# Kernel tuning notes

Measured on AMD Instinct MI355X. Metric: run time of the kernel, lower is better.

Reference implementation:

```python
import jax, jax.numpy as jnp
import numpy as np

EPS = 1e-5      # batch-norm epsilon
ALPHA = 0.2     # leaky_relu negative slope


def bn_lrelu(h, gamma, beta):
    # training-mode batch norm over the batch axis, then leaky relu
    mean = jnp.mean(h, axis=0)
    var = jnp.var(h, axis=0)
    h = (h - mean) * jax.lax.rsqrt(var + EPS) * gamma + beta
    return jnp.where(h >= 0, h, ALPHA * h)


def setup_inputs() -> dict:
    key = jax.random.key(0)
    ks = jax.random.split(key, 16)
    O, T, Din, H, Dout = 50000, 200000, 128, 512, 128
    s = 0.02
    inp = {
        "obj_vecs": jax.random.normal(ks[0], (O, Din), jnp.float32),
        "pred_vecs": jax.random.normal(ks[1], (T, Din), jnp.float32),
        "edges": jax.random.randint(ks[2], (T, 2), 0, O, jnp.int64),
        # net1: [3*Din -> H -> 2H+Dout], each Linear followed by BN + leaky_relu
        "W1a": jax.random.normal(ks[3], (3 * Din, H), jnp.float32) * s,
        "b1a": jnp.zeros((H,), jnp.float32),
        "g1a": jnp.ones((H,), jnp.float32),
        "be1a": jnp.zeros((H,), jnp.float32),
        "W1b": jax.random.normal(ks[4], (H, 2 * H + Dout), jnp.float32) * s,
        "b1b": jnp.zeros((2 * H + Dout,), jnp.float32),
        "g1b": jnp.ones((2 * H + Dout,), jnp.float32),
        "be1b": jnp.zeros((2 * H + Dout,), jnp.float32),
        # net2: [H -> H -> Dout]
        "W2a": jax.random.normal(ks[5], (H, H), jnp.float32) * s,
        "b2a": jnp.zeros((H,), jnp.float32),
        "g2a": jnp.ones((H,), jnp.float32),
        "be2a": jnp.zeros((H,), jnp.float32),
        "W2b": jax.random.normal(ks[6], (H, Dout), jnp.float32) * s,
        "b2b": jnp.zeros((Dout,), jnp.float32),
        "g2b": jnp.ones((Dout,), jnp.float32),
        "be2b": jnp.zeros((Dout,), jnp.float32),
    }
    return inp


def reference(obj_vecs, pred_vecs, edges,
              W1a, b1a, g1a, be1a, W1b, b1b, g1b, be1b,
              W2a, b2a, g2a, be2a, W2b, b2b, g2b, be2b):
    O = obj_vecs.shape[0]
    H = W1a.shape[1]
    Dout = W2b.shape[1]
    s_idx = edges[:, 0]
    o_idx = edges[:, 1]

    # gather subject/object vecs and concat with predicate vecs: [T, 3*Din]
    cur_t = jnp.concatenate([obj_vecs[s_idx], pred_vecs, obj_vecs[o_idx]], axis=1)

    # net1 MLP
    h = bn_lrelu(cur_t @ W1a + b1a, g1a, be1a)           # [T, H]
    new_t = bn_lrelu(h @ W1b + b1b, g1b, be1b)            # [T, 2H+Dout]

    new_s = new_t[:, :H]
    new_p = new_t[:, H:H + Dout]
    new_o = new_t[:, H + Dout:]

    # scatter-add pooling back to objects, then average
    pooled = jnp.zeros((O, H), jnp.float32).at[s_idx].add(new_s).at[o_idx].add(new_o)
    counts = jnp.zeros((O,), jnp.float32).at[s_idx].add(1.0).at[o_idx].add(1.0)
    counts = jnp.clip(counts, 1.0, float(O))
    pooled = pooled / counts[:, None]

    # net2 MLP
    h2 = bn_lrelu(pooled @ W2a + b2a, g2a, be2a)          # [O, H]
    new_obj = bn_lrelu(h2 @ W2b + b2b, g2b, be2b)         # [O, Dout]
    return new_obj, new_p
```

## Files before the change

### kernel.cpp

```cpp
#include <hip/hip_runtime.h>

typedef __bf16 bf16;
typedef __bf16 bf16x4 __attribute__((ext_vector_type(4)));
typedef __bf16 bf16x8 __attribute__((ext_vector_type(8)));
typedef float  f32x4  __attribute__((ext_vector_type(4)));

#define BM 128
#define BN 128
#define BKT 64
#define LDT 72

#ifndef __has_builtin
#define __has_builtin(x) 0
#endif

#if __has_builtin(__builtin_amdgcn_global_load_lds)
#define GLL16(srcp, basep) \
  __builtin_amdgcn_global_load_lds( \
      (const __attribute__((address_space(1))) unsigned int*)(srcp), \
      (__attribute__((address_space(3))) unsigned int*)(basep), 16, 0, 0)
#else
#define GLL16(srcp, basep) \
  (((bf16x8*)(basep))[lane] = *(const bf16x8*)(srcp))
#endif

template<int AMODE, int EPI>
__global__ __launch_bounds__(256) void gemm_k(
    const bf16* __restrict__ Abf, const float* __restrict__ Af32,
    const float* __restrict__ obj, const float* __restrict__ pred,
    const int* __restrict__ edges, const float* __restrict__ invcnt,
    const float* __restrict__ scale, const float* __restrict__ shift,
    const float* __restrict__ oscale, const float* __restrict__ oshift,
    const bf16* __restrict__ WT,
    bf16* __restrict__ outB, float* __restrict__ outF,
    float* __restrict__ pooled, float* __restrict__ gsum, float* __restrict__ gsq,
    int M, int N, int K, int rbase)
{
  __shared__ __align__(16) bf16 As[BM * 64];
  __shared__ __align__(16) bf16 Bs[BN * 64];
  __shared__ float sc_sh[(AMODE == 1) ? 512 : 1];
  __shared__ float sh_sh[(AMODE == 1) ? 512 : 1];
  __shared__ float osc[(EPI == 2 || EPI == 5) ? BN : 1];
  __shared__ float osh[(EPI == 2 || EPI == 5) ? BN : 1];
  __shared__ int eS[(AMODE == 0 || EPI == 2) ? BM : 1];
  __shared__ int eO[(AMODE == 0 || EPI == 2) ? BM : 1];

  const int tid = threadIdx.x;

  int bx = blockIdx.x, by = blockIdx.y;
  {
    const int NX = gridDim.x, NY = gridDim.y;
    int L = by * NX + bx;
    int bpg = NX * 8;
    int nFull = NY >> 3;
    int Lfull = nFull * bpg;
    if (L < Lfull) {
      int g = L / bpg, w2 = L - g * bpg;
      by = (g << 3) + (w2 & 7);
      bx = w2 >> 3;
    } else {
      int r2 = L - Lfull;
      int q = r2 / NX;
      by = (nFull << 3) + q;
      bx = r2 - q * NX;
    }
  }
  const int m0 = rbase + by * BM;
  const int n0 = bx * BN;

  const int lane = tid & 63;
  const int w = tid >> 6;
  const int wm = (w >> 1) * 64;
  const int wn = (w & 1) * 64;
  const int l15 = lane & 15;
  const int quad = lane >> 4;

  if (AMODE == 1) {
    for (int c = tid; c < K; c += 256) { sc_sh[c] = scale[c]; sh_sh[c] = shift[c]; }
  }
  if (EPI == 2 || EPI == 5) {
    if (tid < BN) { osc[tid] = oscale[n0 + tid]; osh[tid] = oshift[n0 + tid]; }
  }
  if (AMODE == 0 || EPI == 2) {
    if (tid < BM) {
      int r = m0 + tid; if (r >= M) r = M - 1;
      eS[tid] = edges[2 * r];
      eO[tid] = edges[2 * r + 1];
    }
  }
  __syncthreads();

  f32x4 acc[4][4];
  #pragma unroll
  for (int i = 0; i < 4; ++i)
    #pragma unroll
    for (int j = 0; j < 4; ++j)
      acc[i][j] = (f32x4){0.f, 0.f, 0.f, 0.f};

  const int rsub = lane >> 3;
  const int cch  = lane & 7;

  for (int k0 = 0; k0 < K; k0 += BKT) {
    #pragma unroll
    for (int it = 0; it < 4; ++it) {
      int blk = it * 4 + w;
      int r = blk * 8 + rsub;
      int cs = cch ^ (r & 7);
      const bf16* src = WT + (size_t)(n0 + r) * K + k0 + cs * 8;
      GLL16(src, &Bs[blk * 512]);
    }
    if (AMODE == 3) {
      #pragma unroll
      for (int it = 0; it < 4; ++it) {
        int blk = it * 4 + w;
        int r = blk * 8 + rsub;
        int row = m0 + r; if (row >= M) row = M - 1;
        int cs = cch ^ (r & 7);
        const bf16* src = Abf + (size_t)row * K + k0 + cs * 8;
        GLL16(src, &As[blk * 512]);
      }
    } else if (AMODE == 1) {
      int idx = tid;
      #pragma unroll
      for (int it = 0; it < 4; ++it, idx += 256) {
        int r = idx >> 3, ch = idx & 7;
        int row = m0 + r; if (row >= M) row = M - 1;
        bf16x8 v = *reinterpret_cast<const bf16x8*>(Abf + (size_t)row * K + k0 + ch * 8);
        bf16x8 o;
        #pragma unroll
        for (int e = 0; e < 8; ++e) {
          int c = k0 + ch * 8 + e;
          float f = sc_sh[c] * (float)v[e] + sh_sh[c];
          f = f >= 0.f ? f : 0.2f * f;
          o[e] = (bf16)f;
        }
        *reinterpret_cast<bf16x8*>(&As[r * 64 + ((ch ^ (r & 7)) << 3)]) = o;
      }
    } else {
      int idx = tid;
      #pragma unroll
      for (int it = 0; it < 8; ++it, idx += 256) {
        int r = idx >> 4, c4 = (idx & 15) << 2;
        int row = m0 + r; if (row >= M) row = M - 1;
        const float* src;
        float mul = 1.f;
        if (AMODE == 0) {
          int k = k0 + c4;
          if (k < 128)      src = obj  + (size_t)eS[r] * 128 + k;
          else if (k < 256) src = pred + (size_t)row * 128 + (k - 128);
          else              src = obj  + (size_t)eO[r] * 128 + (k - 256);
        } else {
          src = Af32 + (size_t)row * K + k0 + c4;
          mul = invcnt[row];
        }
        float4 v = *reinterpret_cast<const float4*>(src);
        bf16x4 o;
        o[0] = (bf16)(v.x * mul); o[1] = (bf16)(v.y * mul);
        o[2] = (bf16)(v.z * mul); o[3] = (bf16)(v.w * mul);
        int ch = c4 >> 3;
        int half = (c4 >> 2) & 1;
        *reinterpret_cast<bf16x4*>(&As[r * 64 + ((ch ^ (r & 7)) << 3) + (half << 2)]) = o;
      }
    }
    __syncthreads();
    #pragma unroll
    for (int kk = 0; kk < BKT; kk += 32) {
      bf16x8 af[4], bfv[4];
      #pragma unroll
      for (int i = 0; i < 4; ++i) {
        int r = wm + i * 16 + l15;
        int ci = (kk >> 3) + quad;
        af[i] = *reinterpret_cast<const bf16x8*>(&As[r * 64 + ((ci ^ (r & 7)) << 3)]);
      }
      #pragma unroll
      for (int j = 0; j < 4; ++j) {
        int r = wn + j * 16 + l15;
        int ci = (kk >> 3) + quad;
        bfv[j] = *reinterpret_cast<const bf16x8*>(&Bs[r * 64 + ((ci ^ (r & 7)) << 3)]);
      }
      #pragma unroll
      for (int i = 0; i < 4; ++i)
        #pragma unroll
        for (int j = 0; j < 4; ++j)
          acc[i][j] = __builtin_amdgcn_mfma_f32_16x16x32_bf16(af[i], bfv[j], acc[i][j], 0, 0, 0);
    }
    __syncthreads();
  }

  if (EPI == 2) {
    #pragma unroll
    for (int i = 0; i < 4; ++i) {
      #pragma unroll
      for (int r = 0; r < 4; ++r) {
        int lrow = wm + i * 16 + quad * 4 + r;
        int row = m0 + lrow;
        if (row >= M) continue;
        #pragma unroll
        for (int j = 0; j < 4; ++j) {
          int cl = wn + j * 16 + l15;
          int n1 = n0 + cl;
          float v = osc[cl] * acc[i][j][r] + osh[cl];
          v = v >= 0.f ? v : 0.2f * v;
          if (n1 < 512)      atomicAdd(&pooled[(size_t)eS[lrow] * 512 + n1], v);
          else if (n1 < 640) outF[(size_t)row * 128 + (n1 - 512)] = v;
          else               atomicAdd(&pooled[(size_t)eO[lrow] * 512 + (n1 - 640)], v);
        }
      }
    }
  } else if (EPI == 5) {
    #pragma unroll
    for (int i = 0; i < 4; ++i) {
      #pragma unroll
      for (int r = 0; r < 4; ++r) {
        int lrow = wm + i * 16 + quad * 4 + r;
        int row = m0 + lrow;
        if (row >= M) continue;
        #pragma unroll
        for (int j = 0; j < 4; ++j) {
          int cl = wn + j * 16 + l15;
          int n1 = n0 + cl;
          float v = osc[cl] * acc[i][j][r] + osh[cl];
          v = v >= 0.f ? v : 0.2f * v;
          if (n1 < 512)      outB[(size_t)(row - rbase) * 1024 + n1] = (bf16)v;
          else if (n1 < 640) outF[(size_t)row * 128 + (n1 - 512)] = v;
          else               outB[(size_t)(row - rbase) * 1024 + (n1 - 128)] = (bf16)v;
        }
      }
    }
  } else {
    #pragma unroll
    for (int j = 0; j < 4; ++j) {
      float s = 0.f, q = 0.f;
      #pragma unroll
      for (int i = 0; i < 4; ++i) {
        #pragma unroll
        for (int r = 0; r < 4; ++r) {
          int row = m0 + wm + i * 16 + quad * 4 + r;
          if (row >= M) continue;
          float v = acc[i][j][r];
          s += v; q += v * v;
          int col = n0 + wn + j * 16 + l15;
          if (EPI == 0) outB[(size_t)row * N + col] = (bf16)v;
          if (EPI == 3) outF[(size_t)row * N + col] = v;
        }
      }
      s += __shfl_xor(s, 16); q += __shfl_xor(q, 16);
      s += __shfl_xor(s, 32); q += __shfl_xor(q, 32);
      if (quad == 0) {
        int col = n0 + wn + j * 16 + l15;
        atomicAdd(&gsum[col], s);
        atomicAdd(&gsq[col], q);
      }
    }
  }
}

__global__ __launch_bounds__(256) void gatherc_k(const bf16* __restrict__ buf,
    const int* __restrict__ rowptr, const int* __restrict__ list,
    float* __restrict__ pooled, int c0, int c1, int O) {
  int o = blockIdx.x * 4 + (threadIdx.x >> 6);
  if (o >= O) return;
  int lane = threadIdx.x & 63;
  int cc = lane * 8;
  int e0 = rowptr[o], e1 = rowptr[o + 1];
  float acc[8];
  #pragma unroll
  for (int j = 0; j < 8; ++j) acc[j] = 0.f;
  bool any = false;
  for (int e = e0; e < e1; ++e) {
    int id = list[e];
    int t = id >> 1;
    if (t < c0 || t >= c1) continue;
    const bf16* row = buf + (size_t)(t - c0) * 1024 + (id & 1) * 512 + cc;
    bf16x8 v = *reinterpret_cast<const bf16x8*>(row);
    #pragma unroll
    for (int j = 0; j < 8; ++j) acc[j] += (float)v[j];
    any = true;
  }
  if (!any) return;
  float* dst = pooled + (size_t)o * 512 + cc;
  float4 a = *reinterpret_cast<float4*>(dst);
  float4 b = *reinterpret_cast<float4*>(dst + 4);
  a.x += acc[0]; a.y += acc[1]; a.z += acc[2]; a.w += acc[3];
  b.x += acc[4]; b.y += acc[5]; b.z += acc[6]; b.w += acc[7];
  *reinterpret_cast<float4*>(dst) = a;
  *reinterpret_cast<float4*>(dst + 4) = b;
}

__global__ __launch_bounds__(256) void gram_k(const bf16* __restrict__ A2,
                                              float* __restrict__ G, int T) {
  __shared__ __align__(16) bf16 Ks[2][128][LDT];
  const int tid = threadIdx.x;
  const int tile = blockIdx.x % 10;
  const int s    = blockIdx.x / 10;
  const int NS   = gridDim.x / 10;
  const int K1T[10] = {0, 0, 0, 0, 1, 1, 1, 2, 2, 3};
  const int K2T[10] = {0, 1, 2, 3, 1, 2, 3, 2, 3, 3};
  const int k1b = K1T[tile], k2b = K2T[tile];
  const int lane = tid & 63;
  const int w = tid >> 6;
  const int wm = (w >> 1) * 64;
  const int wn = (w & 1) * 64;
  const int l15 = lane & 15;
  const int quad = lane >> 4;

  const int NG = (T + 63) >> 6;
  const int GPB = (NG + NS - 1) / NS;
  const int g0 = s * GPB;
  const int gend = min(NG, g0 + GPB);

  f32x4 acc[4][4];
  #pragma unroll
  for (int i = 0; i < 4; ++i)
    #pragma unroll
    for (int j = 0; j < 4; ++j)
      acc[i][j] = (f32x4){0.f, 0.f, 0.f, 0.f};

  const int bsel = (k1b == k2b) ? 0 : 1;

  for (int g = g0; g < gend; ++g) {
    const int t0 = g << 6;
    #pragma unroll
    for (int it = 0; it < 4; ++it) {
      int lin = it * 256 + tid;
      int t = lin >> 4, c8 = lin & 15;
      int row = t0 + t;
      bf16x8 v;
      #pragma unroll
      for (int e = 0; e < 8; ++e) v[e] = (bf16)0.f;
      if (row < T)
        v = *reinterpret_cast<const bf16x8*>(A2 + (size_t)row * 512 + k1b * 128 + c8 * 8);
      int ts = t ^ ((c8 & 7) << 3);
      #pragma unroll
      for (int e = 0; e < 8; ++e) Ks[0][c8 * 8 + e][ts] = v[e];
    }
    if (bsel) {
      #pragma unroll
      for (int it = 0; it < 4; ++it) {
        int lin = it * 256 + tid;
        int t = lin >> 4, c8 = lin & 15;
        int row = t0 + t;
        bf16x8 v;
        #pragma unroll
        for (int e = 0; e < 8; ++e) v[e] = (bf16)0.f;
        if (row < T)
          v = *reinterpret_cast<const bf16x8*>(A2 + (size_t)row * 512 + k2b * 128 + c8 * 8);
        int ts = t ^ ((c8 & 7) << 3);
        #pragma unroll
        for (int e = 0; e < 8; ++e) Ks[1][c8 * 8 + e][ts] = v[e];
      }
    }
    __syncthreads();
    #pragma unroll
    for (int kk = 0; kk < 64; kk += 32) {
      bf16x8 af[4], bfv[4];
      #pragma unroll
      for (int i = 0; i < 4; ++i) {
        int r = wm + i * 16 + l15;
        int toff = (kk + quad * 8) ^ (((r >> 3) & 7) << 3);
        af[i] = *reinterpret_cast<const bf16x8*>(&Ks[0][r][toff]);
      }
      #pragma unroll
      for (int j = 0; j < 4; ++j) {
        int r = wn + j * 16 + l15;
        int toff = (kk + quad * 8) ^ (((r >> 3) & 7) << 3);
        bfv[j] = *reinterpret_cast<const bf16x8*>(&Ks[bsel][r][toff]);
      }
      #pragma unroll
      for (int i = 0; i < 4; ++i)
        #pragma unroll
        for (int j = 0; j < 4; ++j)
          acc[i][j] = __builtin_amdgcn_mfma_f32_16x16x32_bf16(af[i], bfv[j], acc[i][j], 0, 0, 0);
    }
    __syncthreads();
  }

  #pragma unroll
  for (int i = 0; i < 4; ++i) {
    #pragma unroll
    for (int r = 0; r < 4; ++r) {
      int grow = k1b * 128 + wm + i * 16 + quad * 4 + r;
      #pragma unroll
      for (int j = 0; j < 4; ++j) {
        int gcol = k2b * 128 + wn + j * 16 + l15;
        float v = acc[i][j][r];
        atomicAdd(&G[(size_t)grow * 512 + gcol], v);
        if (k1b != k2b)
          atomicAdd(&G[(size_t)gcol * 512 + grow], v);
      }
    }
  }
}

__global__ __launch_bounds__(256) void act_colsum_k(bf16* __restrict__ hA,
    const float* __restrict__ scale, const float* __restrict__ shift,
    float* __restrict__ csum, int T) {
  __shared__ float sh[4 * 512];
  const int tid = threadIdx.x;
  const int c0 = (tid & 63) * 8;
  const int rofs = tid >> 6;
  float sc[8], sf[8];
  #pragma unroll
  for (int j = 0; j < 8; ++j) { sc[j] = scale[c0 + j]; sf[j] = shift[c0 + j]; }
  float acc[8];
  #pragma unroll
  for (int j = 0; j < 8; ++j) acc[j] = 0.f;
  for (int r = blockIdx.x * 4 + rofs; r < T; r += gridDim.x * 4) {
    bf16x8 v = *reinterpret_cast<const bf16x8*>(hA + (size_t)r * 512 + c0);
    bf16x8 o;
    #pragma unroll
    for (int j = 0; j < 8; ++j) {
      float f = sc[j] * (float)v[j] + sf[j];
      f = f >= 0.f ? f : 0.2f * f;
      o[j] = (bf16)f;
      acc[j] += (float)o[j];
    }
    *reinterpret_cast<bf16x8*>(hA + (size_t)r * 512 + c0) = o;
  }
  #pragma unroll
  for (int j = 0; j < 8; ++j) sh[rofs * 512 + c0 + j] = acc[j];
  __syncthreads();
  for (int c = tid; c < 512; c += 256) {
    float s = sh[c] + sh[512 + c] + sh[1024 + c] + sh[1536 + c];
    atomicAdd(&csum[c], s);
  }
}

__global__ __launch_bounds__(256) void colstat_k(const float* __restrict__ G,
    const float* __restrict__ csum, const float* __restrict__ W1b,
    float* __restrict__ sumB, float* __restrict__ sqB) {
  __shared__ float wL[4][512];
  __shared__ float rq[4][4], rs[4][4];
  const int tid = threadIdx.x;
  const int c0 = blockIdx.x * 4;
  for (int idx = tid; idx < 2048; idx += 256) {
    int c = idx >> 9, k = idx & 511;
    wL[c][k] = W1b[(size_t)k * 1152 + c0 + c];
  }
  __syncthreads();
  float pq[4] = {0.f, 0.f, 0.f, 0.f};
  float ps[4] = {0.f, 0.f, 0.f, 0.f};
  for (int e = tid; e < 512 * 512; e += 256) {
    int i = e >> 9, j = e & 511;
    float g = G[e];
    #pragma unroll
    for (int c = 0; c < 4; ++c) pq[c] += g * wL[c][i] * wL[c][j];
  }
  for (int k = tid; k < 512; k += 256) {
    float cs = csum[k];
    #pragma unroll
    for (int c = 0; c < 4; ++c) ps[c] += cs * wL[c][k];
  }
  #pragma unroll
  for (int c = 0; c < 4; ++c) {
    #pragma unroll
    for (int off = 32; off > 0; off >>= 1) {
      pq[c] += __shfl_xor(pq[c], off);
      ps[c] += __shfl_xor(ps[c], off);
    }
  }
  const int w = tid >> 6, lane = tid & 63;
  if (lane == 0) {
    #pragma unroll
    for (int c = 0; c < 4; ++c) { rq[w][c] = pq[c]; rs[w][c] = ps[c]; }
  }
  __syncthreads();
  if (tid < 4) {
    sqB[c0 + tid]  = rq[0][tid] + rq[1][tid] + rq[2][tid] + rq[3][tid];
    sumB[c0 + tid] = rs[0][tid] + rs[1][tid] + rs[2][tid] + rs[3][tid];
  }
}

__global__ __launch_bounds__(256) void tconv_k(const float* __restrict__ W,
                                               bf16* __restrict__ WT, int K, int N) {
  int idx = blockIdx.x * 256 + threadIdx.x;
  if (idx < K * N) {
    int n = idx / K, k = idx - n * K;
    WT[(size_t)n * K + k] = (bf16)W[(size_t)k * N + n];
  }
}

__global__ __launch_bounds__(256) void bnfin_k(const float* __restrict__ sum,
    const float* __restrict__ sq, const float* __restrict__ g,
    const float* __restrict__ be, float* __restrict__ scale,
    float* __restrict__ shift, int C, float invR) {
  int c = blockIdx.x * 256 + threadIdx.x;
  if (c < C) {
    float m = sum[c] * invR;
    float v = sq[c] * invR - m * m;
    float a = g[c] * rsqrtf(v + 1e-5f);
    scale[c] = a;
    shift[c] = be[c] - m * a;
  }
}

__global__ __launch_bounds__(256) void cntint_k(const int* __restrict__ edges,
                                                int* __restrict__ cnt, int T) {
  int t = blockIdx.x * 256 + threadIdx.x;
  if (t < T) {
    atomicAdd(&cnt[edges[2 * t]], 1);
    atomicAdd(&cnt[edges[2 * t + 1]], 1);
  }
}

__global__ __launch_bounds__(256) void invcnt_k(const int* __restrict__ cnt,
                                                float* __restrict__ invc, int O) {
  int i = blockIdx.x * 256 + threadIdx.x;
  if (i < O) {
    float c = fminf(fmaxf((float)cnt[i], 1.f), (float)O);
    invc[i] = 1.f / c;
  }
}

__global__ __launch_bounds__(1024) void scan_k(const int* __restrict__ cnt,
    int* __restrict__ rowptr, int* __restrict__ head, int O, int total) {
  __shared__ int sh[1024];
  const int t = threadIdx.x;
  const int C = (O + 1023) / 1024;
  const int i0 = t * C;
  int s = 0;
  for (int i = 0; i < C; ++i) { int idx = i0 + i; if (idx < O) s += cnt[idx]; }
  sh[t] = s;
  __syncthreads();
  for (int d = 1; d < 1024; d <<= 1) {
    int v = (t >= d) ? sh[t - d] : 0;
    __syncthreads();
    sh[t] += v;
    __syncthreads();
  }
  int run = (t == 0) ? 0 : sh[t - 1];
  for (int i = 0; i < C; ++i) {
    int idx = i0 + i;
    if (idx < O) { rowptr[idx] = run; head[idx] = run; run += cnt[idx]; }
  }
  if (t == 0) rowptr[O] = total;
}

__global__ __launch_bounds__(256) void fill_k(const int* __restrict__ edges,
    int* __restrict__ head, int* __restrict__ list, int T) {
  int t = blockIdx.x * 256 + threadIdx.x;
  if (t < T) {
    int s = edges[2 * t];
    int p = atomicAdd(&head[s], 1);
    list[p] = t << 1;
    int o = edges[2 * t + 1];
    p = atomicAdd(&head[o], 1);
    list[p] = (t << 1) | 1;
  }
}

__global__ __launch_bounds__(256) void final_k(float* __restrict__ buf,
    const float* __restrict__ scale, const float* __restrict__ shift, int n) {
  int i = blockIdx.x * 256 + threadIdx.x;
  if (i < n) {
    int c = i & 127;
    float v = scale[c] * buf[i] + shift[c];
    buf[i] = v >= 0.f ? v : 0.2f * v;
  }
}

extern "C" void kernel_launch(void* const* d_in, const int* in_sizes, int n_in,
                              void* d_out, int out_size, void* d_ws, size_t ws_size,
                              hipStream_t stream) {
  const float* obj   = (const float*)d_in[0];
  const float* pred  = (const float*)d_in[1];
  const int*   edges = (const int*)d_in[2];
  const float* W1a = (const float*)d_in[3];
  const float* g1a = (const float*)d_in[5];
  const float* be1a= (const float*)d_in[6];
  const float* W1b = (const float*)d_in[7];
  const float* g1b = (const float*)d_in[9];
  const float* be1b= (const float*)d_in[10];
  const float* W2a = (const float*)d_in[11];
  const float* g2a = (const float*)d_in[13];
  const float* be2a= (const float*)d_in[14];
  const float* W2b = (const float*)d_in[15];
  const float* g2b = (const float*)d_in[17];
  const float* be2b= (const float*)d_in[18];

  const int O = in_sizes[0] / 128;
  const int T = in_sizes[1] / 128;
  float* out_obj = (float*)d_out;
  float* out_p   = (float*)d_out + (size_t)O * 128;

  char* base = (char*)d_ws;
  size_t off = 0;
  auto alloc = [&](size_t bytes) { size_t p = off; off += (bytes + 255) & ~(size_t)255; return p; };
  size_t oWT1a = alloc((size_t)384 * 512 * 2);
  size_t oWT1b = alloc((size_t)512 * 1152 * 2);
  size_t oWT2a = alloc((size_t)512 * 512 * 2);
  size_t oWT2b = alloc((size_t)512 * 128 * 2);
  size_t oSums = alloc(4608 * 4);
  size_t oScl  = alloc(4608 * 4);
  size_t oG    = alloc((size_t)512 * 512 * 4);
  size_t oCsum = alloc(512 * 4);
  size_t oCnt  = alloc((size_t)O * 4);
  size_t oInvc = alloc((size_t)O * 4);
  size_t oRp   = alloc((size_t)(O + 1) * 4);
  size_t oHead = alloc((size_t)O * 4);
  size_t oList = alloc((size_t)2 * T * 4);
  size_t oHA   = alloc((size_t)T * 512 * 2);
  size_t oPool = off;
  size_t oBuf  = oPool + (((size_t)O * 512 * 4 + 255) & ~(size_t)255);

  int chunkT = 0;
  if (ws_size > oBuf) {
    size_t ct = (ws_size - oBuf) / 2048;
    if (ct > (size_t)T) ct = T;
    chunkT = (int)(ct & ~(size_t)127);
  }
  const bool chunked = (chunkT >= 8192);

  bf16* WT1a = (bf16*)(base + oWT1a);
  bf16* WT1b = (bf16*)(base + oWT1b);
  bf16* WT2a = (bf16*)(base + oWT2a);
  bf16* WT2b = (bf16*)(base + oWT2b);
  float* sums = (float*)(base + oSums);
  float* sumA = sums,        * sqA = sums + 512;
  float* sumB = sums + 1024, * sqB = sums + 2176;
  float* sumC = sums + 3328, * sqC = sums + 3840;
  float* sumD = sums + 4352, * sqD = sums + 4480;
  float* scl = (float*)(base + oScl);
  float* scaleA = scl,        * shiftA = scl + 512;
  float* scaleB = scl + 1024, * shiftB = scl + 2176;
  float* scaleC = scl + 3328, * shiftC = scl + 3840;
  float* scaleD = scl + 4352, * shiftD = scl + 4480;
  float* Gm   = (float*)(base + oG);
  float* csum = (float*)(base + oCsum);
  int*   cntI = (int*)(base + oCnt);
  float* invc = (float*)(base + oInvc);
  int*   rowptr = (int*)(base + oRp);
  int*   head = (int*)(base + oHead);
  int*   list = (int*)(base + oList);
  bf16*  hA = (bf16*)(base + oHA);
  bf16*  h2 = (bf16*)(base + oHA);
  float* pooledF = (float*)(base + oPool);
  bf16*  buf = (bf16*)(base + oBuf);
  float* objpre = out_obj;

  hipMemsetAsync(sums, 0, 4608 * 4, stream);
  hipMemsetAsync(cntI, 0, (size_t)O * 4, stream);
  hipMemsetAsync(Gm, 0, (size_t)512 * 512 * 4, stream);
  hipMemsetAsync(csum, 0, 512 * 4, stream);
  hipMemsetAsync(pooledF, 0, (size_t)O * 512 * 4, stream);

  tconv_k<<<(384 * 512 + 255) / 256, 256, 0, stream>>>(W1a, WT1a, 384, 512);
  tconv_k<<<(512 * 1152 + 255) / 256, 256, 0, stream>>>(W1b, WT1b, 512, 1152);
  tconv_k<<<(512 * 512 + 255) / 256, 256, 0, stream>>>(W2a, WT2a, 512, 512);
  tconv_k<<<(512 * 128 + 255) / 256, 256, 0, stream>>>(W2b, WT2b, 512, 128);
  cntint_k<<<(T + 255) / 256, 256, 0, stream>>>(edges, cntI, T);
  invcnt_k<<<(O + 255) / 256, 256, 0, stream>>>(cntI, invc, O);
  if (chunked) {
    scan_k<<<1, 1024, 0, stream>>>(cntI, rowptr, head, O, 2 * T);
    fill_k<<<(T + 255) / 256, 256, 0, stream>>>(edges, head, list, T);
  }

  const int Tb = (T + BM - 1) / BM;
  const int Ob = (O + BM - 1) / BM;

  {
    dim3 g(512 / BN, Tb);
    gemm_k<0, 0><<<g, 256, 0, stream>>>(nullptr, nullptr, obj, pred, edges, nullptr,
        nullptr, nullptr, nullptr, nullptr, WT1a, hA, nullptr, nullptr, sumA, sqA,
        T, 512, 384, 0);
  }
  bnfin_k<<<2, 256, 0, stream>>>(sumA, sqA, g1a, be1a, scaleA, shiftA, 512, 1.f / T);

  act_colsum_k<<<1024, 256, 0, stream>>>(hA, scaleA, shiftA, csum, T);
  gram_k<<<10 * 48, 256, 0, stream>>>(hA, Gm, T);
  colstat_k<<<288, 256, 0, stream>>>(Gm, csum, W1b, sumB, sqB);
  bnfin_k<<<5, 256, 0, stream>>>(sumB, sqB, g1b, be1b, scaleB, shiftB, 1152, 1.f / T);

  if (chunked) {
    for (int c0 = 0; c0 < T; c0 += chunkT) {
      int c1 = min(T, c0 + chunkT);
      dim3 g(1152 / BN, (c1 - c0 + BM - 1) / BM);
      gemm_k<3, 5><<<g, 256, 0, stream>>>(hA, nullptr, nullptr, nullptr, nullptr,
          nullptr, nullptr, nullptr, scaleB, shiftB, WT1b, buf, out_p, nullptr,
          nullptr, nullptr, c1, 1152, 512, c0);
      gatherc_k<<<(O + 3) / 4, 256, 0, stream>>>(buf, rowptr, list, pooledF, c0, c1, O);
    }
  } else {
    dim3 g(1152 / BN, Tb);
    gemm_k<3, 2><<<g, 256, 0, stream>>>(hA, nullptr, nullptr, nullptr, edges, nullptr,
        nullptr, nullptr, scaleB, shiftB, WT1b, nullptr, out_p, pooledF, nullptr,
        nullptr, T, 1152, 512, 0);
  }

  {
    dim3 g(512 / BN, Ob);
    gemm_k<2, 0><<<g, 256, 0, stream>>>(nullptr, pooledF, nullptr, nullptr, nullptr,
        invc, nullptr, nullptr, nullptr, nullptr, WT2a, h2, nullptr, nullptr,
        sumC, sqC, O, 512, 512, 0);
  }
  bnfin_k<<<2, 256, 0, stream>>>(sumC, sqC, g2a, be2a, scaleC, shiftC, 512, 1.f / O);

  {
    dim3 g(128 / BN, Ob);
    gemm_k<1, 3><<<g, 256, 0, stream>>>(h2, nullptr, nullptr, nullptr, nullptr, nullptr,
        scaleC, shiftC, nullptr, nullptr, WT2b, nullptr, objpre, nullptr, sumD, sqD,
        O, 128, 512, 0);
  }
  bnfin_k<<<1, 256, 0, stream>>>(sumD, sqD, g2b, be2b, scaleD, shiftD, 128, 1.f / O);

  final_k<<<((size_t)O * 128 + 255) / 256, 256, 0, stream>>>(objpre, scaleD, shiftD,
      (int)((size_t)O * 128));
}
```

Before: 2.028 ms.

## Pre-convert inputs to bf16 for async LDS gather loads and split BN column-stat kernel

Adds kernels that convert obj/pred vectors to bf16 up front, so the first GEMM can gather rows straight into LDS with global_load_lds (new AMODE 5) instead of loading fp32 and converting inside the kernel. Pooled features are also scaled by the inverse count and converted to bf16 before the net2 GEMM, which then uses the direct-load path. The column-statistics kernel is split across 8x more blocks with float4 reads and atomics, and the sum term moves to a separate kernel. This costs extra conversion passes and workspace, and depends on the workspace being large enough.

```diff
diff --git a/kernel.cpp b/kernel.cpp
--- a/kernel.cpp
+++ b/kernel.cpp
@@ -42,8 +42,8 @@
   __shared__ float sh_sh[(AMODE == 1) ? 512 : 1];
   __shared__ float osc[(EPI == 2 || EPI == 5) ? BN : 1];
   __shared__ float osh[(EPI == 2 || EPI == 5) ? BN : 1];
-  __shared__ int eS[(AMODE == 0 || EPI == 2) ? BM : 1];
-  __shared__ int eO[(AMODE == 0 || EPI == 2) ? BM : 1];
+  __shared__ int eS[(AMODE == 0 || AMODE == 5 || EPI == 2) ? BM : 1];
+  __shared__ int eO[(AMODE == 0 || AMODE == 5 || EPI == 2) ? BM : 1];
 
   const int tid = threadIdx.x;
 
@@ -81,7 +81,7 @@
   if (EPI == 2 || EPI == 5) {
     if (tid < BN) { osc[tid] = oscale[n0 + tid]; osh[tid] = oshift[n0 + tid]; }
   }
-  if (AMODE == 0 || EPI == 2) {
+  if (AMODE == 0 || AMODE == 5 || EPI == 2) {
     if (tid < BM) {
       int r = m0 + tid; if (r >= M) r = M - 1;
       eS[tid] = edges[2 * r];
@@ -117,6 +117,22 @@
         int row = m0 + r; if (row >= M) row = M - 1;
         int cs = cch ^ (r & 7);
         const bf16* src = Abf + (size_t)row * K + k0 + cs * 8;
+        GLL16(src, &As[blk * 512]);
+      }
+    } else if (AMODE == 5) {
+      const bf16* objB  = (const bf16*)obj;
+      const bf16* predB = (const bf16*)pred;
+      #pragma unroll
+      for (int it = 0; it < 4; ++it) {
+        int blk = it * 4 + w;
+        int r = blk * 8 + rsub;
+        int row = m0 + r; if (row >= M) row = M - 1;
+        int cs = cch ^ (r & 7);
+        int k = k0 + cs * 8;
+        const bf16* src;
+        if (k0 < 128)      src = objB  + (size_t)eS[r] * 128 + k;
+        else if (k0 < 256) src = predB + (size_t)row * 128 + (k - 128);
+        else               src = objB  + (size_t)eO[r] * 128 + (k - 256);
         GLL16(src, &As[blk * 512]);
       }
     } else if (AMODE == 1) {
@@ -255,6 +271,222 @@
   }
 }
 
+__global__ __launch_bounds__(256) void convf2b_k(const float* __restrict__ src,
+    bf16* __restrict__ dst, size_t n8) {
+  size_t i = (size_t)blockIdx.x * 256 + threadIdx.x;
+  if (i < n8) {
+    const float4* s = reinterpret_cast<const float4*>(src + i * 8);
+    float4 a = s[0], b = s[1];
+    bf16x8 o;
+    o[0] = (bf16)a.x; o[1] = (bf16)a.y; o[2] = (bf16)a.z; o[3] = (bf16)a.w;
+    o[4] = (bf16)b.x; o[5] = (bf16)b.y; o[6] = (bf16)b.z; o[7] = (bf16)b.w;
+    reinterpret_cast<bf16x8*>(dst)[i] = o;
+  }
+}
+
+__global__ __launch_bounds__(256) void pconv_k(const float* __restrict__ pooledF,
+    const float* __restrict__ invc, bf16* __restrict__ pooledB, int O) {
+  size_t i = (size_t)blockIdx.x * 256 + threadIdx.x;
+  if (i < (size_t)O * 64) {
+    int o = (int)(i >> 6);
+    float ic = invc[o];
+    const float4* s = reinterpret_cast<const float4*>(pooledF + i * 8);
+    float4 a = s[0], b = s[1];
+    bf16x8 v;
+    v[0] = (bf16)(a.x * ic); v[1] = (bf16)(a.y * ic);
+    v[2] = (bf16)(a.z * ic); v[3] = (bf16)(a.w * ic);
+    v[4] = (bf16)(b.x * ic); v[5] = (bf16)(b.y * ic);
+    v[6] = (bf16)(b.z * ic); v[7] = (bf16)(b.w * ic);
+    reinterpret_cast<bf16x8*>(pooledB)[i] = v;
+  }
+}
+
+__global__ __launch_bounds__(256) void gram_k(const bf16* __restrict__ A2,
+                                              float* __restrict__ G, int T) {
+  __shared__ __align__(16) bf16 Ks[2][128][LDT];
+  const int tid = threadIdx.x;
+  const int tile = blockIdx.x % 10;
+  const int s    = blockIdx.x / 10;
+  const int NS   = gridDim.x / 10;
+  const int K1T[10] = {0, 0, 0, 0, 1, 1, 1, 2, 2, 3};
+  const int K2T[10] = {0, 1, 2, 3, 1, 2, 3, 2, 3, 3};
+  const int k1b = K1T[tile], k2b = K2T[tile];
+  const int lane = tid & 63;
+  const int w = tid >> 6;
+  const int wm = (w >> 1) * 64;
+  const int wn = (w & 1) * 64;
+  const int l15 = lane & 15;
+  const int quad = lane >> 4;
+  const int NG = (T + 63) >> 6;
+  const int GPB = (NG + NS - 1) / NS;
+  const int g0 = s * GPB;
+  const int gend = min(NG, g0 + GPB);
+  f32x4 acc[4][4];
+  #pragma unroll
+  for (int i = 0; i < 4; ++i)
+    #pragma unroll
+    for (int j = 0; j < 4; ++j)
+      acc[i][j] = (f32x4){0.f, 0.f, 0.f, 0.f};
+  const int bsel = (k1b == k2b) ? 0 : 1;
+  for (int g = g0; g < gend; ++g) {
+    const int t0 = g << 6;
+    #pragma unroll
+    for (int it = 0; it < 4; ++it) {
+      int lin = it * 256 + tid;
+      int t = lin >> 4, c8 = lin & 15;
+      int row = t0 + t;
+      bf16x8 v;
+      #pragma unroll
+      for (int e = 0; e < 8; ++e) v[e] = (bf16)0.f;
+      if (row < T)
+        v = *reinterpret_cast<const bf16x8*>(A2 + (size_t)row * 512 + k1b * 128 + c8 * 8);
+      int ts = t ^ ((c8 & 7) << 3);
+      #pragma unroll
+      for (int e = 0; e < 8; ++e) Ks[0][c8 * 8 + e][ts] = v[e];
+    }
+    if (bsel) {
+      #pragma unroll
+      for (int it = 0; it < 4; ++it) {
+        int lin = it * 256 + tid;
+        int t = lin >> 4, c8 = lin & 15;
+        int row = t0 + t;
+        bf16x8 v;
+        #pragma unroll
+        for (int e = 0; e < 8; ++e) v[e] = (bf16)0.f;
+        if (row < T)
+          v = *reinterpret_cast<const bf16x8*>(A2 + (size_t)row * 512 + k2b * 128 + c8 * 8);
+        int ts = t ^ ((c8 & 7) << 3);
+        #pragma unroll
+        for (int e = 0; e < 8; ++e) Ks[1][c8 * 8 + e][ts] = v[e];
+      }
+    }
+    __syncthreads();
+    #pragma unroll
+    for (int kk = 0; kk < 64; kk += 32) {
+      bf16x8 af[4], bfv[4];
+      #pragma unroll
+      for (int i = 0; i < 4; ++i) {
+        int r = wm + i * 16 + l15;
+        int toff = (kk + quad * 8) ^ (((r >> 3) & 7) << 3);
+        af[i] = *reinterpret_cast<const bf16x8*>(&Ks[0][r][toff]);
+      }
+      #pragma unroll
+      for (int j = 0; j < 4; ++j) {
+        int r = wn + j * 16 + l15;
+        int toff = (kk + quad * 8) ^ (((r >> 3) & 7) << 3);
+        bfv[j] = *reinterpret_cast<const bf16x8*>(&Ks[bsel][r][toff]);
+      }
+      #pragma unroll
+      for (int i = 0; i < 4; ++i)
+        #pragma unroll
+        for (int j = 0; j < 4; ++j)
+          acc[i][j] = __builtin_amdgcn_mfma_f32_16x16x32_bf16(af[i], bfv[j], acc[i][j], 0, 0, 0);
+    }
+    __syncthreads();
+  }
+  #pragma unroll
+  for (int i = 0; i < 4; ++i) {
+    #pragma unroll
+    for (int r = 0; r < 4; ++r) {
+      int grow = k1b * 128 + wm + i * 16 + quad * 4 + r;
+      #pragma unroll
+      for (int j = 0; j < 4; ++j) {
+        int gcol = k2b * 128 + wn + j * 16 + l15;
+        float v = acc[i][j][r];
+        atomicAdd(&G[(size_t)grow * 512 + gcol], v);
+        if (k1b != k2b)
+          atomicAdd(&G[(size_t)gcol * 512 + grow], v);
+      }
+    }
+  }
+}
+
+__global__ __launch_bounds__(256) void act_colsum_k(bf16* __restrict__ hA,
+    const float* __restrict__ scale, const float* __restrict__ shift,
+    float* __restrict__ csum, int T) {
+  __shared__ float sh[4 * 512];
+  const int tid = threadIdx.x;
+  const int c0 = (tid & 63) * 8;
+  const int rofs = tid >> 6;
+  float sc[8], sf[8];
+  #pragma unroll
+  for (int j = 0; j < 8; ++j) { sc[j] = scale[c0 + j]; sf[j] = shift[c0 + j]; }
+  float acc[8];
+  #pragma unroll
+  for (int j = 0; j < 8; ++j) acc[j] = 0.f;
+  for (int r = blockIdx.x * 4 + rofs; r < T; r += gridDim.x * 4) {
+    bf16x8 v = *reinterpret_cast<const bf16x8*>(hA + (size_t)r * 512 + c0);
+    bf16x8 o;
+    #pragma unroll
+    for (int j = 0; j < 8; ++j) {
+      float f = sc[j] * (float)v[j] + sf[j];
+      f = f >= 0.f ? f : 0.2f * f;
+      o[j] = (bf16)f;
+      acc[j] += (float)o[j];
+    }
+    *reinterpret_cast<bf16x8*>(hA + (size_t)r * 512 + c0) = o;
+  }
+  #pragma unroll
+  for (int j = 0; j < 8; ++j) sh[rofs * 512 + c0 + j] = acc[j];
+  __syncthreads();
+  for (int c = tid; c < 512; c += 256) {
+    float s = sh[c] + sh[512 + c] + sh[1024 + c] + sh[1536 + c];
+    atomicAdd(&csum[c], s);
+  }
+}
+
+__global__ __launch_bounds__(256) void colstat_k(const float* __restrict__ G,
+    const float* __restrict__ W1b, float* __restrict__ sqB) {
+  __shared__ float wL[4][512];
+  __shared__ float rq[4][4];
+  const int tid = threadIdx.x;
+  const int c0 = (blockIdx.x >> 3) * 4;
+  const int rs = (blockIdx.x & 7) * 64;
+  for (int idx = tid; idx < 2048; idx += 256) {
+    int c = idx >> 9, k = idx & 511;
+    wL[c][k] = W1b[(size_t)k * 1152 + c0 + c];
+  }
+  __syncthreads();
+  float pq[4] = {0.f, 0.f, 0.f, 0.f};
+  #pragma unroll 4
+  for (int v = tid; v < 8192; v += 256) {
+    int i = rs + (v >> 7);
+    int j = (v & 127) << 2;
+    float4 g = *reinterpret_cast<const float4*>(G + (size_t)i * 512 + j);
+    #pragma unroll
+    for (int c = 0; c < 4; ++c) {
+      float d = g.x * wL[c][j] + g.y * wL[c][j + 1]
+              + g.z * wL[c][j + 2] + g.w * wL[c][j + 3];
+      pq[c] += wL[c][i] * d;
+    }
+  }
+  #pragma unroll
+  for (int c = 0; c < 4; ++c) {
+    #pragma unroll
+    for (int off = 32; off > 0; off >>= 1) pq[c] += __shfl_xor(pq[c], off);
+  }
+  const int w = tid >> 6, lane = tid & 63;
+  if (lane == 0) {
+    #pragma unroll
+    for (int c = 0; c < 4; ++c) rq[w][c] = pq[c];
+  }
+  __syncthreads();
+  if (tid < 4)
+    atomicAdd(&sqB[c0 + tid], rq[0][tid] + rq[1][tid] + rq[2][tid] + rq[3][tid]);
+}
+
+__global__ __launch_bounds__(256) void sumb_k(const float* __restrict__ csum,
+    const float* __restrict__ W1b, float* __restrict__ sumB) {
+  int c = (blockIdx.x >> 2) * 256 + threadIdx.x;
+  int k0 = (blockIdx.x & 3) * 128;
+  if (c < 1152) {
+    float s = 0.f;
+    #pragma unroll 4
+    for (int k = k0; k < k0 + 128; ++k) s += csum[k] * W1b[(size_t)k * 1152 + c];
+    atomicAdd(&sumB[c], s);
+  }
+}
+
 __global__ __launch_bounds__(256) void gatherc_k(const bf16* __restrict__ buf,
     const int* __restrict__ rowptr, const int* __restrict__ list,
     float* __restrict__ pooled, int c0, int c1, int O) {
@@ -285,190 +517,6 @@
   b.x += acc[4]; b.y += acc[5]; b.z += acc[6]; b.w += acc[7];
   *reinterpret_cast<float4*>(dst) = a;
   *reinterpret_cast<float4*>(dst + 4) = b;
-}
-
-__global__ __launch_bounds__(256) void gram_k(const bf16* __restrict__ A2,
-                                              float* __restrict__ G, int T) {
-  __shared__ __align__(16) bf16 Ks[2][128][LDT];
-  const int tid = threadIdx.x;
-  const int tile = blockIdx.x % 10;
-  const int s    = blockIdx.x / 10;
-  const int NS   = gridDim.x / 10;
-  const int K1T[10] = {0, 0, 0, 0, 1, 1, 1, 2, 2, 3};
-  const int K2T[10] = {0, 1, 2, 3, 1, 2, 3, 2, 3, 3};
-  const int k1b = K1T[tile], k2b = K2T[tile];
-  const int lane = tid & 63;
-  const int w = tid >> 6;
-  const int wm = (w >> 1) * 64;
-  const int wn = (w & 1) * 64;
-  const int l15 = lane & 15;
-  const int quad = lane >> 4;
-
-  const int NG = (T + 63) >> 6;
-  const int GPB = (NG + NS - 1) / NS;
-  const int g0 = s * GPB;
-  const int gend = min(NG, g0 + GPB);
-
-  f32x4 acc[4][4];
-  #pragma unroll
-  for (int i = 0; i < 4; ++i)
-    #pragma unroll
-    for (int j = 0; j < 4; ++j)
-      acc[i][j] = (f32x4){0.f, 0.f, 0.f, 0.f};
-
-  const int bsel = (k1b == k2b) ? 0 : 1;
-
-  for (int g = g0; g < gend; ++g) {
-    const int t0 = g << 6;
-    #pragma unroll
-    for (int it = 0; it < 4; ++it) {
-      int lin = it * 256 + tid;
-      int t = lin >> 4, c8 = lin & 15;
-      int row = t0 + t;
-      bf16x8 v;
-      #pragma unroll
-      for (int e = 0; e < 8; ++e) v[e] = (bf16)0.f;
-      if (row < T)
-        v = *reinterpret_cast<const bf16x8*>(A2 + (size_t)row * 512 + k1b * 128 + c8 * 8);
-      int ts = t ^ ((c8 & 7) << 3);
-      #pragma unroll
-      for (int e = 0; e < 8; ++e) Ks[0][c8 * 8 + e][ts] = v[e];
-    }
-    if (bsel) {
-      #pragma unroll
-      for (int it = 0; it < 4; ++it) {
-        int lin = it * 256 + tid;
-        int t = lin >> 4, c8 = lin & 15;
-        int row = t0 + t;
-        bf16x8 v;
-        #pragma unroll
-        for (int e = 0; e < 8; ++e) v[e] = (bf16)0.f;
-        if (row < T)
-          v = *reinterpret_cast<const bf16x8*>(A2 + (size_t)row * 512 + k2b * 128 + c8 * 8);
-        int ts = t ^ ((c8 & 7) << 3);
-        #pragma unroll
-        for (int e = 0; e < 8; ++e) Ks[1][c8 * 8 + e][ts] = v[e];
-      }
-    }
-    __syncthreads();
-    #pragma unroll
-    for (int kk = 0; kk < 64; kk += 32) {
-      bf16x8 af[4], bfv[4];
-      #pragma unroll
-      for (int i = 0; i < 4; ++i) {
-        int r = wm + i * 16 + l15;
-        int toff = (kk + quad * 8) ^ (((r >> 3) & 7) << 3);
-        af[i] = *reinterpret_cast<const bf16x8*>(&Ks[0][r][toff]);
-      }
-      #pragma unroll
-      for (int j = 0; j < 4; ++j) {
-        int r = wn + j * 16 + l15;
-        int toff = (kk + quad * 8) ^ (((r >> 3) & 7) << 3);
-        bfv[j] = *reinterpret_cast<const bf16x8*>(&Ks[bsel][r][toff]);
-      }
-      #pragma unroll
-      for (int i = 0; i < 4; ++i)
-        #pragma unroll
-        for (int j = 0; j < 4; ++j)
-          acc[i][j] = __builtin_amdgcn_mfma_f32_16x16x32_bf16(af[i], bfv[j], acc[i][j], 0, 0, 0);
-    }
-    __syncthreads();
-  }
-
-  #pragma unroll
-  for (int i = 0; i < 4; ++i) {
-    #pragma unroll
-    for (int r = 0; r < 4; ++r) {
-      int grow = k1b * 128 + wm + i * 16 + quad * 4 + r;
-      #pragma unroll
-      for (int j = 0; j < 4; ++j) {
-        int gcol = k2b * 128 + wn + j * 16 + l15;
-        float v = acc[i][j][r];
-        atomicAdd(&G[(size_t)grow * 512 + gcol], v);
-        if (k1b != k2b)
-          atomicAdd(&G[(size_t)gcol * 512 + grow], v);
-      }
-    }
-  }
-}
-
-__global__ __launch_bounds__(256) void act_colsum_k(bf16* __restrict__ hA,
-    const float* __restrict__ scale, const float* __restrict__ shift,
-    float* __restrict__ csum, int T) {
-  __shared__ float sh[4 * 512];
-  const int tid = threadIdx.x;
-  const int c0 = (tid & 63) * 8;
-  const int rofs = tid >> 6;
-  float sc[8], sf[8];
-  #pragma unroll
-  for (int j = 0; j < 8; ++j) { sc[j] = scale[c0 + j]; sf[j] = shift[c0 + j]; }
-  float acc[8];
-  #pragma unroll
-  for (int j = 0; j < 8; ++j) acc[j] = 0.f;
-  for (int r = blockIdx.x * 4 + rofs; r < T; r += gridDim.x * 4) {
-    bf16x8 v = *reinterpret_cast<const bf16x8*>(hA + (size_t)r * 512 + c0);
-    bf16x8 o;
-    #pragma unroll
-    for (int j = 0; j < 8; ++j) {
-      float f = sc[j] * (float)v[j] + sf[j];
-      f = f >= 0.f ? f : 0.2f * f;
-      o[j] = (bf16)f;
-      acc[j] += (float)o[j];
-    }
-    *reinterpret_cast<bf16x8*>(hA + (size_t)r * 512 + c0) = o;
-  }
-  #pragma unroll
-  for (int j = 0; j < 8; ++j) sh[rofs * 512 + c0 + j] = acc[j];
-  __syncthreads();
-  for (int c = tid; c < 512; c += 256) {
-    float s = sh[c] + sh[512 + c] + sh[1024 + c] + sh[1536 + c];
-    atomicAdd(&csum[c], s);
-  }
-}
-
-__global__ __launch_bounds__(256) void colstat_k(const float* __restrict__ G,
-    const float* __restrict__ csum, const float* __restrict__ W1b,
-    float* __restrict__ sumB, float* __restrict__ sqB) {
-  __shared__ float wL[4][512];
-  __shared__ float rq[4][4], rs[4][4];
-  const int tid = threadIdx.x;
-  const int c0 = blockIdx.x * 4;
-  for (int idx = tid; idx < 2048; idx += 256) {
-    int c = idx >> 9, k = idx & 511;
-    wL[c][k] = W1b[(size_t)k * 1152 + c0 + c];
-  }
-  __syncthreads();
-  float pq[4] = {0.f, 0.f, 0.f, 0.f};
-  float ps[4] = {0.f, 0.f, 0.f, 0.f};
-  for (int e = tid; e < 512 * 512; e += 256) {
-    int i = e >> 9, j = e & 511;
-    float g = G[e];
-    #pragma unroll
-    for (int c = 0; c < 4; ++c) pq[c] += g * wL[c][i] * wL[c][j];
-  }
-  for (int k = tid; k < 512; k += 256) {
-    float cs = csum[k];
-    #pragma unroll
-    for (int c = 0; c < 4; ++c) ps[c] += cs * wL[c][k];
-  }
-  #pragma unroll
-  for (int c = 0; c < 4; ++c) {
-    #pragma unroll
-    for (int off = 32; off > 0; off >>= 1) {
-      pq[c] += __shfl_xor(pq[c], off);
-      ps[c] += __shfl_xor(ps[c], off);
-    }
-  }
-  const int w = tid >> 6, lane = tid & 63;
-  if (lane == 0) {
-    #pragma unroll
-    for (int c = 0; c < 4; ++c) { rq[w][c] = pq[c]; rs[w][c] = ps[c]; }
-  }
-  __syncthreads();
-  if (tid < 4) {
-    sqB[c0 + tid]  = rq[0][tid] + rq[1][tid] + rq[2][tid] + rq[3][tid];
-    sumB[c0 + tid] = rs[0][tid] + rs[1][tid] + rs[2][tid] + rs[3][tid];
-  }
 }
 
 __global__ __launch_bounds__(256) void tconv_k(const float* __restrict__ W,
@@ -610,6 +658,10 @@
     chunkT = (int)(ct & ~(size_t)127);
   }
   const bool chunked = (chunkT >= 8192);
+
+  size_t objB_sz  = (((size_t)O * 128 * 2) + 255) & ~(size_t)255;
+  size_t predB_sz = (size_t)T * 128 * 2;
+  const bool canConv = chunked && (ws_size >= oBuf + objB_sz + predB_sz);
 
   bf16* WT1a = (bf16*)(base + oWT1a);
   bf16* WT1b = (bf16*)(base + oWT1b);
@@ -634,8 +686,11 @@
   int*   list = (int*)(base + oList);
   bf16*  hA = (bf16*)(base + oHA);
   bf16*  h2 = (bf16*)(base + oHA);
+  bf16*  pooledB = (bf16*)(base + oHA + (size_t)O * 512 * 4);
   float* pooledF = (float*)(base + oPool);
   bf16*  buf = (bf16*)(base + oBuf);
+  bf16*  objB  = (bf16*)(base + oBuf);
+  bf16*  predB = (bf16*)(base + oBuf + objB_sz);
   float* objpre = out_obj;
 
   hipMemsetAsync(sums, 0, 4608 * 4, stream);
@@ -654,21 +709,31 @@
     scan_k<<<1, 1024, 0, stream>>>(cntI, rowptr, head, O, 2 * T);
     fill_k<<<(T + 255) / 256, 256, 0, stream>>>(edges, head, list, T);
   }
+  if (canConv) {
+    convf2b_k<<<(int)(((size_t)O * 16 + 255) / 256), 256, 0, stream>>>(obj, objB, (size_t)O * 16);
+    convf2b_k<<<(int)(((size_t)T * 16 + 255) / 256), 256, 0, stream>>>(pred, predB, (size_t)T * 16);
+  }
 
   const int Tb = (T + BM - 1) / BM;
   const int Ob = (O + BM - 1) / BM;
 
   {
     dim3 g(512 / BN, Tb);
-    gemm_k<0, 0><<<g, 256, 0, stream>>>(nullptr, nullptr, obj, pred, edges, nullptr,
-        nullptr, nullptr, nullptr, nullptr, WT1a, hA, nullptr, nullptr, sumA, sqA,
-        T, 512, 384, 0);
+    if (canConv)
+      gemm_k<5, 0><<<g, 256, 0, stream>>>(nullptr, nullptr, (const float*)objB,
+          (const float*)predB, edges, nullptr, nullptr, nullptr, nullptr, nullptr,
+          WT1a, hA, nullptr, nullptr, sumA, sqA, T, 512, 384, 0);
+    else
+      gemm_k<0, 0><<<g, 256, 0, stream>>>(nullptr, nullptr, obj, pred, edges, nullptr,
+          nullptr, nullptr, nullptr, nullptr, WT1a, hA, nullptr, nullptr, sumA, sqA,
+          T, 512, 384, 0);
   }
   bnfin_k<<<2, 256, 0, stream>>>(sumA, sqA, g1a, be1a, scaleA, shiftA, 512, 1.f / T);
 
   act_colsum_k<<<1024, 256, 0, stream>>>(hA, scaleA, shiftA, csum, T);
   gram_k<<<10 * 48, 256, 0, stream>>>(hA, Gm, T);
-  colstat_k<<<288, 256, 0, stream>>>(Gm, csum, W1b, sumB, sqB);
+  colstat_k<<<288 * 8, 256, 0, stream>>>(Gm, W1b, sqB);
+  sumb_k<<<((1152 + 255) / 256) * 4, 256, 0, stream>>>(csum, W1b, sumB);
   bnfin_k<<<5, 256, 0, stream>>>(sumB, sqB, g1b, be1b, scaleB, shiftB, 1152, 1.f / T);
 
   if (chunked) {
@@ -680,16 +745,21 @@
           nullptr, nullptr, c1, 1152, 512, c0);
       gatherc_k<<<(O + 3) / 4, 256, 0, stream>>>(buf, rowptr, list, pooledF, c0, c1, O);
     }
+    pconv_k<<<(int)(((size_t)O * 64 + 255) / 256), 256, 0, stream>>>(pooledF, invc,
+        pooledB, O);
+    {
+      dim3 g(512 / BN, Ob);
+      gemm_k<3, 0><<<g, 256, 0, stream>>>(pooledB, nullptr, nullptr, nullptr, nullptr,
+          nullptr, nullptr, nullptr, nullptr, nullptr, WT2a, h2, nullptr, nullptr,
+          sumC, sqC, O, 512, 512, 0);
+    }
   } else {
-    dim3 g(1152 / BN, Tb);
-    gemm_k<3, 2><<<g, 256, 0, stream>>>(hA, nullptr, nullptr, nullptr, edges, nullptr,
+    dim3 g2(1152 / BN, Tb);
+    gemm_k<3, 2><<<g2, 256, 0, stream>>>(hA, nullptr, nullptr, nullptr, edges, nullptr,
         nullptr, nullptr, scaleB, shiftB, WT1b, nullptr, out_p, pooledF, nullptr,
         nullptr, T, 1152, 512, 0);
-  }
-
-  {
-    dim3 g(512 / BN, Ob);
-    gemm_k<2, 0><<<g, 256, 0, stream>>>(nullptr, pooledF, nullptr, nullptr, nullptr,
+    dim3 g3(512 / BN, Ob);
+    gemm_k<2, 0><<<g3, 256, 0, stream>>>(nullptr, pooledF, nullptr, nullptr, nullptr,
         invc, nullptr, nullptr, nullptr, nullptr, WT2a, h2, nullptr, nullptr,
         sumC, sqC, O, 512, 512, 0);
   }
```

After: 1.797 ms. 1.13x faster.
